# Kernel tuning notes

Measured on AMD Instinct MI355X. Metric: run time of the kernel, lower is better.

Reference implementation:

```python
import jax, jax.numpy as jnp
import numpy as np

B, N, C_IN, C_OUT, K = 16, 16384, 128, 128, 9


def setup_inputs() -> dict:
    key = jax.random.key(0)
    ks = jax.random.split(key, 7)
    x = jax.random.normal(ks[0], (B, N, C_IN), dtype=jnp.float32)
    indices = jax.random.randint(ks[1], (N, K), 0, N, dtype=jnp.int32)
    # P initialized near identity (as in the torch module) plus small noise
    P = jnp.eye(K, dtype=jnp.float32)[None].repeat(N, axis=0) \
        + 0.02 * jax.random.normal(ks[2], (N, K, K), dtype=jnp.float32)
    W_conv = jax.random.normal(ks[3], (C_OUT, K * C_IN), dtype=jnp.float32) * (1.0 / np.sqrt(K * C_IN))
    b_conv = jax.random.normal(ks[4], (C_OUT,), dtype=jnp.float32) * 0.01
    W_skip = jax.random.normal(ks[5], (C_OUT, C_IN), dtype=jnp.float32) * (1.0 / np.sqrt(C_IN))
    b_skip = jax.random.normal(ks[6], (C_OUT,), dtype=jnp.float32) * 0.01
    return {"x": x, "indices": indices, "P": P, "W_conv": W_conv,
            "b_conv": b_conv, "W_skip": W_skip, "b_skip": b_skip}


def reference(x, indices, P, W_conv, b_conv, W_skip, b_skip):
    b, n, c = x.shape
    k = P.shape[-1]
    # pad node axis with k zero rows (matches x_padded in torch module)
    x_pad = jnp.concatenate([x, jnp.zeros((b, k, c), dtype=x.dtype)], axis=1)
    # gather k neighbours per node: (b, n, k, c)
    nbr = jnp.take(x_pad, indices, axis=1)
    # per-node kxk permutation/mixing matmul: P (n,k,k) @ nbr (b,n,k,c)
    perm = jnp.einsum('nkj,bnjc->bnkc', P, nbr)
    flat = jax.nn.elu(perm.reshape(b, n, k * c))
    z = jax.nn.elu(jnp.einsum('bnf,of->bno', flat, W_conv) + b_conv)
    # skip connection
    z = jnp.einsum('bnc,oc->bno', x, W_skip) + b_skip + z
    return z
```

## Files before the change

### kernel.cpp

```cpp
#include <hip/hip_runtime.h>
#include <hip/hip_fp16.h>
#include <math.h>

#define B_ 16
#define N_ 16384
#define C_ 128
#define K_ 9
#define FCONV 1152
#define G_ 2
#define FPAD 1160
#define LDS_BYTES (G_ * B_ * FPAD * 2)

typedef _Float16 half8 __attribute__((ext_vector_type(8)));
typedef float floatx4 __attribute__((ext_vector_type(4)));

__device__ __forceinline__ float elu_f(float v) {
    return v > 0.f ? v : (__expf(v) - 1.f);
}

__global__ void build_wfrag(const float* __restrict__ Wc, const float* __restrict__ Ws,
                            _Float16* __restrict__ WcF, _Float16* __restrict__ WsF) {
    const int i = blockIdx.x * 256 + threadIdx.x;
    if (i < 8 * 36 * 64 * 8) {
        const int j = i & 7, lane = (i >> 3) & 63;
        const int rest = i >> 9;
        const int kc = rest % 36, ot = rest / 36;
        WcF[i] = (_Float16)Wc[(size_t)(ot * 16 + (lane & 15)) * FCONV + kc * 32 + (lane >> 4) * 8 + j];
    }
    if (i < 8 * 4 * 64 * 8) {
        const int j = i & 7, lane = (i >> 3) & 63;
        const int rest = i >> 9;
        const int kc = rest & 3, ot = rest >> 2;
        WsF[i] = (_Float16)Ws[(size_t)(ot * 16 + (lane & 15)) * C_ + kc * 32 + (lane >> 4) * 8 + j];
    }
}

template <bool WF16>
__global__ __launch_bounds__(1024, 8) void paiconv_mfma(
    const float* __restrict__ x,
    const int*   __restrict__ idx,
    const float* __restrict__ P,
    const void*  __restrict__ WcP,
    const float* __restrict__ bc,
    const void*  __restrict__ WsP,
    const float* __restrict__ bs,
    float*       __restrict__ out)
{
    extern __shared__ _Float16 flat_s[];

    const int tid = threadIdx.x;
    const int n0  = blockIdx.x * G_;

    {
        const int c  = tid & (C_ - 1);
        const int bg = tid >> 7;
        #pragma unroll
        for (int g = 0; g < G_; ++g) {
            const int n = n0 + g;
            int id[K_];
            #pragma unroll
            for (int j = 0; j < K_; ++j) id[j] = idx[(size_t)n * K_ + j];

            float v[2][K_];
            #pragma unroll
            for (int i = 0; i < 2; ++i) {
                const int m = bg * 2 + i;
                const float* xb = x + (size_t)m * (N_ * C_) + c;
                #pragma unroll
                for (int j = 0; j < K_; ++j)
                    v[i][j] = ((unsigned)id[j] < (unsigned)N_) ? xb[(size_t)id[j] * C_] : 0.f;
            }

            _Float16* fg = &flat_s[g * (B_ * FPAD)];
            const float* Pn = P + (size_t)n * 81;
            #pragma unroll
            for (int k = 0; k < K_; ++k) {
                float pr[K_];
                #pragma unroll
                for (int j = 0; j < K_; ++j) pr[j] = Pn[k * K_ + j];
                #pragma unroll
                for (int i = 0; i < 2; ++i) {
                    float s = 0.f;
                    #pragma unroll
                    for (int j = 0; j < K_; ++j) s = fmaf(pr[j], v[i][j], s);
                    fg[(bg * 2 + i) * FPAD + k * C_ + c] = (_Float16)elu_f(s);
                }
            }
        }
    }
    __syncthreads();

    const int w    = tid >> 6;
    const int lane = tid & 63;
    const int col  = lane & 15;
    const int quad = lane >> 4;
    const int g    = w & 1;
    const int ot   = w >> 1;
    const int o0   = ot * 16;
    const int n    = n0 + g;

    floatx4 accC = (floatx4){0.f, 0.f, 0.f, 0.f};
    floatx4 accS = (floatx4){0.f, 0.f, 0.f, 0.f};

    for (int k0 = 0; k0 < C_; k0 += 32) {
        const float* p = x + (size_t)col * (N_ * C_) + (size_t)n * C_ + k0 + quad * 8;
        const float4 x0 = *(const float4*)p;
        const float4 x1 = *(const float4*)(p + 4);
        half8 a = (half8){(_Float16)x0.x, (_Float16)x0.y, (_Float16)x0.z, (_Float16)x0.w,
                          (_Float16)x1.x, (_Float16)x1.y, (_Float16)x1.z, (_Float16)x1.w};
        half8 b;
        if (WF16) {
            b = ((const half8*)WsP)[(ot * 4 + (k0 >> 5)) * 64 + lane];
        } else {
            const float* q = (const float*)WsP + (size_t)(o0 + col) * C_ + k0 + quad * 8;
            const float4 w0 = *(const float4*)q;
            const float4 w1 = *(const float4*)(q + 4);
            b = (half8){(_Float16)w0.x, (_Float16)w0.y, (_Float16)w0.z, (_Float16)w0.w,
                        (_Float16)w1.x, (_Float16)w1.y, (_Float16)w1.z, (_Float16)w1.w};
        }
        accS = __builtin_amdgcn_mfma_f32_16x16x32_f16(a, b, accS, 0, 0, 0);
    }

    const _Float16* fg = &flat_s[g * (B_ * FPAD) + col * FPAD];
    for (int k0 = 0; k0 < FCONV; k0 += 32) {
        half8 a = *(const half8*)&fg[k0 + quad * 8];
        half8 b;
        if (WF16) {
            b = ((const half8*)WcP)[(ot * 36 + (k0 >> 5)) * 64 + lane];
        } else {
            const float* q = (const float*)WcP + (size_t)(o0 + col) * FCONV + k0 + quad * 8;
            const float4 w0 = *(const float4*)q;
            const float4 w1 = *(const float4*)(q + 4);
            b = (half8){(_Float16)w0.x, (_Float16)w0.y, (_Float16)w0.z, (_Float16)w0.w,
                        (_Float16)w1.x, (_Float16)w1.y, (_Float16)w1.z, (_Float16)w1.w};
        }
        accC = __builtin_amdgcn_mfma_f32_16x16x32_f16(a, b, accC, 0, 0, 0);
    }

    const float bcv = bc[o0 + col];
    const float bsv = bs[o0 + col];
    #pragma unroll
    for (int r = 0; r < 4; ++r) {
        const int m = quad * 4 + r;
        const float z = elu_f(accC[r] + bcv);
        __builtin_nontemporal_store(z + accS[r] + bsv,
                                    &out[((size_t)m * N_ + n) * C_ + o0 + col]);
    }
}

extern "C" void kernel_launch(void* const* d_in, const int* in_sizes, int n_in,
                              void* d_out, int out_size, void* d_ws, size_t ws_size,
                              hipStream_t stream) {
    const float* x   = (const float*)d_in[0];
    const int*   idx = (const int*)  d_in[1];
    const float* P   = (const float*)d_in[2];
    const float* Wc  = (const float*)d_in[3];
    const float* bc  = (const float*)d_in[4];
    const float* Ws  = (const float*)d_in[5];
    const float* bs  = (const float*)d_in[6];
    float* out = (float*)d_out;

    const size_t wc_halfs = (size_t)8 * 36 * 64 * 8;
    const size_t ws_halfs = (size_t)8 * 4 * 64 * 8;
    const size_t need = (wc_halfs + ws_halfs) * sizeof(_Float16);

    if (ws_size >= need) {
        _Float16* WcF = (_Float16*)d_ws;
        _Float16* WsF = WcF + wc_halfs;
        build_wfrag<<<dim3(576), dim3(256), 0, stream>>>(Wc, Ws, WcF, WsF);
        hipFuncSetAttribute((const void*)paiconv_mfma<true>,
                            hipFuncAttributeMaxDynamicSharedMemorySize, LDS_BYTES);
        paiconv_mfma<true><<<dim3(N_ / G_), dim3(1024), LDS_BYTES, stream>>>(
            x, idx, P, WcF, bc, WsF, bs, out);
    } else {
        hipFuncSetAttribute((const void*)paiconv_mfma<false>,
                            hipFuncAttributeMaxDynamicSharedMemorySize, LDS_BYTES);
        paiconv_mfma<false><<<dim3(N_ / G_), dim3(1024), LDS_BYTES, stream>>>(
            x, idx, P, Wc, bc, Ws, bs, out);
    }
}
```

Baseline: 598.5 us.

## Pre-convert x to fp16 in a prep pass and gather half2 pairs per thread

```diff
diff --git a/kernel.cpp b/kernel.cpp
--- a/kernel.cpp
+++ b/kernel.cpp
@@ -12,10 +12,42 @@
 #define LDS_BYTES (G_ * B_ * FPAD * 2)
 
 typedef _Float16 half8 __attribute__((ext_vector_type(8)));
+typedef _Float16 half2v __attribute__((ext_vector_type(2)));
 typedef float floatx4 __attribute__((ext_vector_type(4)));
 
 __device__ __forceinline__ float elu_f(float v) {
     return v > 0.f ? v : (__expf(v) - 1.f);
+}
+
+__global__ __launch_bounds__(1024) void prep(
+    const float* __restrict__ x, const float* __restrict__ Wc, const float* __restrict__ Ws,
+    _Float16* __restrict__ x16, _Float16* __restrict__ WcF, _Float16* __restrict__ WsF)
+{
+    const int t = blockIdx.x * 1024 + threadIdx.x;
+    const int NX8 = B_ * N_ * C_ / 8;
+    if (t < NX8) {
+        const float4 a = ((const float4*)x)[(size_t)t * 2];
+        const float4 b = ((const float4*)x)[(size_t)t * 2 + 1];
+        half8 h = {(_Float16)a.x, (_Float16)a.y, (_Float16)a.z, (_Float16)a.w,
+                   (_Float16)b.x, (_Float16)b.y, (_Float16)b.z, (_Float16)b.w};
+        *(half8*)(x16 + (size_t)t * 8) = h;
+    } else {
+        const int i = t - NX8;
+        if (i < 8 * 36 * 64 * 8) {
+            const int j = i & 7, lane = (i >> 3) & 63;
+            const int rest = i >> 9;
+            const int kc = rest % 36, ot = rest / 36;
+            WcF[i] = (_Float16)Wc[(size_t)(ot * 16 + (lane & 15)) * FCONV + kc * 32 + (lane >> 4) * 8 + j];
+        } else {
+            const int i2 = i - 8 * 36 * 64 * 8;
+            if (i2 < 8 * 4 * 64 * 8) {
+                const int j = i2 & 7, lane = (i2 >> 3) & 63;
+                const int rest = i2 >> 9;
+                const int kc = rest & 3, ot = rest >> 2;
+                WsF[i2] = (_Float16)Ws[(size_t)(ot * 16 + (lane & 15)) * C_ + kc * 32 + (lane >> 4) * 8 + j];
+            }
+        }
+    }
 }
 
 __global__ void build_wfrag(const float* __restrict__ Wc, const float* __restrict__ Ws,
@@ -35,16 +67,17 @@
     }
 }
 
-template <bool WF16>
+template <bool XF16, bool WF16>
 __global__ __launch_bounds__(1024, 8) void paiconv_mfma(
-    const float* __restrict__ x,
-    const int*   __restrict__ idx,
-    const float* __restrict__ P,
-    const void*  __restrict__ WcP,
-    const float* __restrict__ bc,
-    const void*  __restrict__ WsP,
-    const float* __restrict__ bs,
-    float*       __restrict__ out)
+    const float*    __restrict__ x,
+    const _Float16* __restrict__ x16,
+    const int*      __restrict__ idx,
+    const float*    __restrict__ P,
+    const void*     __restrict__ WcP,
+    const float*    __restrict__ bc,
+    const void*     __restrict__ WsP,
+    const float*    __restrict__ bs,
+    float*          __restrict__ out)
 {
     extern __shared__ _Float16 flat_s[];
 
@@ -52,8 +85,8 @@
     const int n0  = blockIdx.x * G_;
 
     {
-        const int c  = tid & (C_ - 1);
-        const int bg = tid >> 7;
+        const int cp = tid & 63;
+        const int m  = tid >> 6;
         #pragma unroll
         for (int g = 0; g < G_; ++g) {
             const int n = n0 + g;
@@ -61,30 +94,34 @@
             #pragma unroll
             for (int j = 0; j < K_; ++j) id[j] = idx[(size_t)n * K_ + j];
 
-            float v[2][K_];
+            float vx[K_], vy[K_];
             #pragma unroll
-            for (int i = 0; i < 2; ++i) {
-                const int m = bg * 2 + i;
-                const float* xb = x + (size_t)m * (N_ * C_) + c;
-                #pragma unroll
-                for (int j = 0; j < K_; ++j)
-                    v[i][j] = ((unsigned)id[j] < (unsigned)N_) ? xb[(size_t)id[j] * C_] : 0.f;
+            for (int j = 0; j < K_; ++j) {
+                const bool ok = (unsigned)id[j] < (unsigned)N_;
+                if (XF16) {
+                    const _Float16* q = x16 + ((size_t)m * N_ + id[j]) * C_ + 2 * cp;
+                    half2v h = ok ? *(const half2v*)q : (half2v){(_Float16)0.f, (_Float16)0.f};
+                    vx[j] = (float)h[0]; vy[j] = (float)h[1];
+                } else {
+                    const float* q = x + ((size_t)m * N_ + id[j]) * C_ + 2 * cp;
+                    float2 h = ok ? *(const float2*)q : (float2){0.f, 0.f};
+                    vx[j] = h.x; vy[j] = h.y;
+                }
             }
 
-            _Float16* fg = &flat_s[g * (B_ * FPAD)];
             const float* Pn = P + (size_t)n * 81;
+            _Float16* fg = &flat_s[g * (B_ * FPAD) + m * FPAD + 2 * cp];
             #pragma unroll
             for (int k = 0; k < K_; ++k) {
-                float pr[K_];
+                float s0 = 0.f, s1 = 0.f;
                 #pragma unroll
-                for (int j = 0; j < K_; ++j) pr[j] = Pn[k * K_ + j];
-                #pragma unroll
-                for (int i = 0; i < 2; ++i) {
-                    float s = 0.f;
-                    #pragma unroll
-                    for (int j = 0; j < K_; ++j) s = fmaf(pr[j], v[i][j], s);
-                    fg[(bg * 2 + i) * FPAD + k * C_ + c] = (_Float16)elu_f(s);
+                for (int j = 0; j < K_; ++j) {
+                    const float p = Pn[k * K_ + j];
+                    s0 = fmaf(p, vx[j], s0);
+                    s1 = fmaf(p, vy[j], s1);
                 }
+                half2v r = {(_Float16)elu_f(s0), (_Float16)elu_f(s1)};
+                *(half2v*)&fg[k * C_] = r;
             }
         }
     }
@@ -103,11 +140,16 @@
     floatx4 accS = (floatx4){0.f, 0.f, 0.f, 0.f};
 
     for (int k0 = 0; k0 < C_; k0 += 32) {
-        const float* p = x + (size_t)col * (N_ * C_) + (size_t)n * C_ + k0 + quad * 8;
-        const float4 x0 = *(const float4*)p;
-        const float4 x1 = *(const float4*)(p + 4);
-        half8 a = (half8){(_Float16)x0.x, (_Float16)x0.y, (_Float16)x0.z, (_Float16)x0.w,
-                          (_Float16)x1.x, (_Float16)x1.y, (_Float16)x1.z, (_Float16)x1.w};
+        half8 a;
+        if (XF16) {
+            a = *(const half8*)(x16 + ((size_t)col * N_ + n) * C_ + k0 + quad * 8);
+        } else {
+            const float* p = x + ((size_t)col * N_ + n) * C_ + k0 + quad * 8;
+            const float4 x0 = *(const float4*)p;
+            const float4 x1 = *(const float4*)(p + 4);
+            a = (half8){(_Float16)x0.x, (_Float16)x0.y, (_Float16)x0.z, (_Float16)x0.w,
+                        (_Float16)x1.x, (_Float16)x1.y, (_Float16)x1.z, (_Float16)x1.w};
+        }
         half8 b;
         if (WF16) {
             b = ((const half8*)WsP)[(ot * 4 + (k0 >> 5)) * 64 + lane];
@@ -160,22 +202,33 @@
     const float* bs  = (const float*)d_in[6];
     float* out = (float*)d_out;
 
-    const size_t wc_halfs = (size_t)8 * 36 * 64 * 8;
-    const size_t ws_halfs = (size_t)8 * 4 * 64 * 8;
-    const size_t need = (wc_halfs + ws_halfs) * sizeof(_Float16);
-
-    if (ws_size >= need) {
+    const size_t x16_halfs = (size_t)B_ * N_ * C_;
+    const size_t wc_halfs  = (size_t)8 * 36 * 64 * 8;
+    const size_t wsk_halfs = (size_t)8 * 4 * 64 * 8;
+    const size_t need_full = (x16_halfs + wc_halfs + wsk_halfs) * sizeof(_Float16);
+    const size_t need_w    = (wc_halfs + wsk_halfs) * sizeof(_Float16);
+
+    if (ws_size >= need_full) {
+        _Float16* x16 = (_Float16*)d_ws;
+        _Float16* WcF = x16 + x16_halfs;
+        _Float16* WsF = WcF + wc_halfs;
+        prep<<<dim3(4256), dim3(1024), 0, stream>>>(x, Wc, Ws, x16, WcF, WsF);
+        hipFuncSetAttribute((const void*)paiconv_mfma<true, true>,
+                            hipFuncAttributeMaxDynamicSharedMemorySize, LDS_BYTES);
+        paiconv_mfma<true, true><<<dim3(N_ / G_), dim3(1024), LDS_BYTES, stream>>>(
+            x, x16, idx, P, WcF, bc, WsF, bs, out);
+    } else if (ws_size >= need_w) {
         _Float16* WcF = (_Float16*)d_ws;
         _Float16* WsF = WcF + wc_halfs;
         build_wfrag<<<dim3(576), dim3(256), 0, stream>>>(Wc, Ws, WcF, WsF);
-        hipFuncSetAttribute((const void*)paiconv_mfma<true>,
+        hipFuncSetAttribute((const void*)paiconv_mfma<false, true>,
                             hipFuncAttributeMaxDynamicSharedMemorySize, LDS_BYTES);
-        paiconv_mfma<true><<<dim3(N_ / G_), dim3(1024), LDS_BYTES, stream>>>(
-            x, idx, P, WcF, bc, WsF, bs, out);
+        paiconv_mfma<false, true><<<dim3(N_ / G_), dim3(1024), LDS_BYTES, stream>>>(
+            x, nullptr, idx, P, WcF, bc, WsF, bs, out);
     } else {
-        hipFuncSetAttribute((const void*)paiconv_mfma<false>,
+        hipFuncSetAttribute((const void*)paiconv_mfma<false, false>,
                             hipFuncAttributeMaxDynamicSharedMemorySize, LDS_BYTES);
-        paiconv_mfma<false><<<dim3(N_ / G_), dim3(1024), LDS_BYTES, stream>>>(
-            x, idx, P, Wc, bc, Ws, bs, out);
-    }
-}
+        paiconv_mfma<false, false><<<dim3(N_ / G_), dim3(1024), LDS_BYTES, stream>>>(
+            x, nullptr, idx, P, Wc, bc, Ws, bs, out);
+    }
+}
```

Measured after the change: 605.6 us. No clear change (+1.2%).
